# Kernel optimization log

Hardware: AMD Instinct MI355X
Metric: run time of the kernel (lower is better)

The kernel has to match this reference:

```python
import jax, jax.numpy as jnp
import numpy as np

EPS_MIN = 1e-8
N_ITER = 50  # solver_iter


def solve_qp_simplex(M, n_iter=N_ITER):
    """Frank-Wolfe min over the simplex of alpha^T M alpha. M: (B,K,K) -> alpha: (B,K)."""
    B, K, _ = M.shape
    alpha0 = jnp.full((B, K), 1.0 / K, dtype=M.dtype)

    def step(alpha, it):
        grad = 2.0 * jnp.einsum('bij,bj->bi', M, alpha)           # (B,K)
        idx = jnp.argmin(grad, axis=1)                             # (B,)
        s = jax.nn.one_hot(idx, K, dtype=alpha.dtype)              # vertex of simplex
        gamma = 2.0 / (it + 2.0)
        return (1.0 - gamma) * alpha + gamma * s, None

    alpha, _ = jax.lax.scan(step, alpha0, jnp.arange(n_iter, dtype=M.dtype))
    return alpha


def _raw_loss(scores, targets, C):
    B, K = scores.shape
    # epsilon = offdiag_mean of C per batch, scaled by 1.0, clamped
    offdiag_mean = (C.sum(axis=(1, 2)) - jnp.trace(C, axis1=1, axis2=2)) / (K * K - K)
    eps = jnp.maximum(offdiag_mean, EPS_MIN)                       # (B,)

    f = 0.5 * scores
    exponent = -(f[:, :, None] + f[:, None, :] + C) / eps[:, None, None]  # (B,K,K)
    shift = exponent.max(axis=(1, 2), keepdims=True)
    logM = exponent - shift
    M = jnp.exp(logM)

    # solver is an implicit layer: non-differentiable by construction
    alpha = jax.lax.stop_gradient(solve_qp_simplex(M, N_ITER))     # (B,K)

    pos = alpha > 0
    loga = jnp.where(pos, jnp.log(jnp.where(pos, alpha, 1.0)), -jnp.inf)
    term = loga[:, :, None] + loga[:, None, :] + logM              # (B,K,K)
    logval = jax.scipy.special.logsumexp(term.reshape(B, K * K), axis=1)
    conjugate = -eps * (logval + shift.reshape(B))

    f_y = jnp.take_along_axis(scores, targets[:, None], axis=1)[:, 0]
    return conjugate - f_y


def setup_inputs() -> dict:
    key = jax.random.key(0)
    k1, k2, k3 = jax.random.split(key, 3)
    B, K = 512, 256
    scores = jax.random.normal(k1, (B, K), dtype=jnp.float32)
    targets = jax.random.randint(k2, (B,), 0, K)
    C = jax.random.uniform(k3, (B, K, K), dtype=jnp.float32)
    return {"scores": scores, "targets": targets, "C": C}


def reference(scores, targets, C):
    return _raw_loss(scores, targets, C).mean()
```

## Files before the change

### kernel.cpp

```cpp
#include <hip/hip_runtime.h>
#include <math.h>

#define KDIM 256
#define NITER 50


__global__ __launch_bounds__(256) void k1_partials(
    const float* __restrict__ scores, const float* __restrict__ C,
    float* __restrict__ psum_o, float* __restrict__ ptrace_o, float* __restrict__ pmin_o)
{
    const int blk = blockIdx.x;
    const int b = blk >> 2, chunk = blk & 3;
    const int tid = threadIdx.x, lane = tid & 63, wave = tid >> 6;
    const float4* C4 = (const float4*)(C + (size_t)b * KDIM * KDIM);

    __shared__ float4 sf4[KDIM/4];
    __shared__ float redS[256], redT[256], redM[256];
    const float* sf = (const float*)sf4;
    ((float*)sf4)[tid] = 0.5f * scores[b*KDIM + tid];
    __syncthreads();

    const int row0 = chunk * 64;
    float psum = 0.f, ptrace = 0.f, pmin = INFINITY;
    #pragma unroll
    for (int rr = 0; rr < 16; ++rr) {
        const int row = row0 + wave + rr*4;
        float4 c4 = C4[row*(KDIM/4) + lane];
        float frow = sf[row];
        float4 fj = sf4[lane];
        psum += (c4.x + c4.y) + (c4.z + c4.w);
        pmin = fminf(pmin, fminf(fminf(frow+fj.x+c4.x, frow+fj.y+c4.y),
                                 fminf(frow+fj.z+c4.z, frow+fj.w+c4.w)));
        if ((row >> 2) == lane) {
            int r2 = row & 3;
            ptrace += (r2==0) ? c4.x : (r2==1) ? c4.y : (r2==2) ? c4.z : c4.w;
        }
    }
    redS[tid] = psum; redT[tid] = ptrace; redM[tid] = pmin;
    __syncthreads();
    for (int s = 128; s > 0; s >>= 1) {
        if (tid < s) {
            redS[tid] += redS[tid+s];
            redT[tid] += redT[tid+s];
            redM[tid]  = fminf(redM[tid], redM[tid+s]);
        }
        __syncthreads();
    }
    if (tid == 0) { psum_o[blk] = redS[0]; ptrace_o[blk] = redT[0]; pmin_o[blk] = redM[0]; }
}

__global__ __launch_bounds__(256) void k2_grad0(
    const float* __restrict__ scores, const float* __restrict__ C,
    const float* __restrict__ psum_i, const float* __restrict__ ptrace_i, const float* __restrict__ pmin_i,
    float* __restrict__ rsval_o, int* __restrict__ rsidx_o)
{
    const int blk = blockIdx.x;
    const int b = blk >> 2, chunk = blk & 3;
    const int tid = threadIdx.x, lane = tid & 63, wave = tid >> 6;
    const float4* C4 = (const float4*)(C + (size_t)b * KDIM * KDIM);

    __shared__ float4 sf4[KDIM/4];
    __shared__ float rs64[64];
    const float* sf = (const float*)sf4;
    ((float*)sf4)[tid] = 0.5f * scores[b*KDIM + tid];
    __syncthreads();

    float sum = 0.f, tr = 0.f, mn = INFINITY;
    #pragma unroll
    for (int c2 = 0; c2 < 4; ++c2) {
        sum += psum_i[b*4 + c2];
        tr  += ptrace_i[b*4 + c2];
        mn   = fminf(mn, pmin_i[b*4 + c2]);
    }
    const float eps = fmaxf((sum - tr) / (float)(KDIM*KDIM - KDIM), 1e-8f);
    const float inv_eps = 1.0f / eps;
    const float minv = mn;

    const int row0 = chunk * 64;
    for (int rr = wave; rr < 64; rr += 4) {
        const int row = row0 + rr;
        float4 c4 = C4[row*(KDIM/4) + lane];
        float frow = sf[row];
        float4 fj = sf4[lane];
        float p = __expf((minv - (frow+fj.x+c4.x)) * inv_eps)
                + __expf((minv - (frow+fj.y+c4.y)) * inv_eps)
                + __expf((minv - (frow+fj.z+c4.z)) * inv_eps)
                + __expf((minv - (frow+fj.w+c4.w)) * inv_eps);
        for (int off = 32; off > 0; off >>= 1) p += __shfl_xor(p, off);
        if (lane == 0) rs64[rr] = p;
    }
    __syncthreads();
    if (wave == 0) {
        float v = rs64[lane]; int vi = row0 + lane;
        for (int off = 32; off > 0; off >>= 1) {
            float ov = __shfl_xor(v, off);
            int  ovi = __shfl_xor(vi, off);
            if (ov < v || (ov == v && ovi < vi)) { v = ov; vi = ovi; }
        }
        if (lane == 0) { rsval_o[blk] = v; rsidx_o[blk] = vi; }
    }
}

__global__ __launch_bounds__(256) void k3_fw(
    const float* __restrict__ scores, const int* __restrict__ targets,
    const float* __restrict__ C,
    const float* __restrict__ psum_i, const float* __restrict__ ptrace_i, const float* __restrict__ pmin_i,
    const float* __restrict__ rsval_i, const int* __restrict__ rsidx_i,
    float* __restrict__ lossB)
{
    const int b = blockIdx.x;
    const int tid = threadIdx.x, lane = tid & 63, wave = tid >> 6;
    const float* Cb = C + (size_t)b * KDIM * KDIM;

    __shared__ float4 sf4[KDIM/4];
    __shared__ float red[KDIM];
    __shared__ float rs[KDIM];
    __shared__ float wmin[4];
    __shared__ int   widx[4];
    __shared__ int   wcnt[4];
    __shared__ int   sIdx[64];
    __shared__ float sLog[64];

    const float* sf = (const float*)sf4;
    ((float*)sf4)[tid] = 0.5f * scores[b*KDIM + tid];
    __syncthreads();

    float sum = 0.f, tr = 0.f, mn = INFINITY;
    #pragma unroll
    for (int c2 = 0; c2 < 4; ++c2) {
        sum += psum_i[b*4 + c2];
        tr  += ptrace_i[b*4 + c2];
        mn   = fminf(mn, pmin_i[b*4 + c2]);
    }
    const float eps = fmaxf((sum - tr) / (float)(KDIM*KDIM - KDIM), 1e-8f);
    const float inv_eps = 1.0f / eps;
    const float minv = mn;

    float bv = INFINITY; int idx0 = 0;
    #pragma unroll
    for (int c2 = 0; c2 < 4; ++c2) {
        float v = rsval_i[b*4 + c2];
        int  vi = rsidx_i[b*4 + c2];
        if (v < bv) { bv = v; idx0 = vi; }
    }

    const float fi = sf[tid];
    float a = (tid == idx0) ? 1.0f : 0.0f;
    {
        const float c = Cb[tid*KDIM + idx0];
        float dummy; (void)dummy;
        a = a;
    }
    float g;
    {
        const float c = Cb[tid*KDIM + idx0];
        g = 2.0f * __expf((minv - (fi + sf[idx0] + c)) * inv_eps);
    }

    for (int it = 1; it < NITER; ++it) {
        float v = g; int vi = tid;
        for (int off = 32; off > 0; off >>= 1) {
            float ov = __shfl_xor(v, off);
            int  ovi = __shfl_xor(vi, off);
            if (ov < v || (ov == v && ovi < vi)) { v = ov; vi = ovi; }
        }
        if (lane == 0) { wmin[wave] = v; widx[wave] = vi; }
        __syncthreads();
        float cbv = wmin[0]; int cbi = widx[0];
        #pragma unroll
        for (int w = 1; w < 4; ++w) {
            float wv = wmin[w]; int wi = widx[w];
            if (wv < cbv || (wv == cbv && wi < cbi)) { cbv = wv; cbi = wi; }
        }
        const int idx = cbi;
        const float gamma = 2.0f / ((float)it + 2.0f);
        const float fidx = sf[idx];
        const float c = Cb[tid*KDIM + idx];
        const float mcol = __expf((minv - (fi + fidx + c)) * inv_eps);
        g = (1.0f - gamma)*g + 2.0f*gamma*mcol;
        a = (1.0f - gamma)*a + ((tid == idx) ? gamma : 0.0f);
        __syncthreads();
    }

    unsigned long long mask = __ballot(a > 0.f);
    if (lane == 0) wcnt[wave] = __popcll(mask);
    __syncthreads();
    int off0 = 0;
    for (int w = 0; w < wave; ++w) off0 += wcnt[w];
    const int count = wcnt[0] + wcnt[1] + wcnt[2] + wcnt[3];
    if (a > 0.f) {
        int pos = off0 + __popcll(mask & ((1ull << lane) - 1ull));
        sIdx[pos] = tid;
        sLog[pos] = logf(a);
    }
    __syncthreads();

    float m = -INFINITY, ss = 0.f;
    const int total = count * count;
    for (int p = tid; p < total; p += KDIM) {
        int ii = p / count;
        int jj = p - ii * count;
        int i = sIdx[ii], j = sIdx[jj];
        float cij = Cb[i*KDIM + j];
        float lm = (minv - (sf[i] + sf[j] + cij)) * inv_eps;
        float t = sLog[ii] + sLog[jj] + lm;
        if (t > m) { ss = ss * __expf(m - t) + 1.0f; m = t; }
        else       { ss += __expf(t - m); }
    }
    red[tid] = m; rs[tid] = ss;
    __syncthreads();
    for (int s = 128; s > 0; s >>= 1) {
        if (tid < s) {
            float m1 = red[tid],   s1 = rs[tid];
            float m2 = red[tid+s], s2 = rs[tid+s];
            if (s2 > 0.f) {
                if (s1 <= 0.f)    { red[tid] = m2; rs[tid] = s2; }
                else if (m2 > m1) { red[tid] = m2; rs[tid] = s1*__expf(m1-m2) + s2; }
                else              { rs[tid] = s1 + s2*__expf(m2-m1); }
            }
        }
        __syncthreads();
    }
    if (tid == 0) {
        float logval = red[0] + logf(rs[0]);
        float shift = -minv * inv_eps;
        float conjugate = -eps * (logval + shift);
        float fy = scores[b*KDIM + targets[b]];
        lossB[b] = conjugate - fy;
    }
}

__global__ __launch_bounds__(512) void cacis_reduce(const float* __restrict__ lossB,
                                                    float* __restrict__ out, int B)
{
    __shared__ float red[512];
    int t = threadIdx.x;
    red[t] = (t < B) ? lossB[t] : 0.f;
    __syncthreads();
    for (int s = 256; s > 0; s >>= 1) { if (t < s) red[t] += red[t+s]; __syncthreads(); }
    if (t == 0) out[0] = red[0] / (float)B;
}

extern "C" void kernel_launch(void* const* d_in, const int* in_sizes, int n_in,
                              void* d_out, int out_size, void* d_ws, size_t ws_size,
                              hipStream_t stream) {
    const float* scores  = (const float*)d_in[0];
    const int*   targets = (const int*)d_in[1];
    const float* C       = (const float*)d_in[2];
    float* out = (float*)d_out;
    const int B = in_sizes[1];

    float* ws     = (float*)d_ws;
    float* psum   = ws;
    float* ptrace = ws + 2048;
    float* pmin   = ws + 4096;
    float* rsval  = ws + 6144;
    int*   rsidx  = (int*)(ws + 8192);
    float* lossB  = ws + 10240;

    k1_partials<<<B*4, 256, 0, stream>>>(scores, C, psum, ptrace, pmin);
    k2_grad0   <<<B*4, 256, 0, stream>>>(scores, C, psum, ptrace, pmin, rsval, rsidx);
    k3_fw      <<<B,   256, 0, stream>>>(scores, targets, C, psum, ptrace, pmin, rsval, rsidx, lossB);
    cacis_reduce<<<1, 512, 0, stream>>>(lossB, out, B);
}
```

Baseline: 121.4 us.

## Run Frank-Wolfe loop in a single wave and use shuffle-based logsumexp reduction

The 49-iteration Frank-Wolfe loop now runs in one 64-lane wave, with each lane holding four rows. The per-iteration argmin needs only wave shuffles, which removes two block-wide barriers and the shared-memory cross-wave step from every iteration. The final logsumexp merge also switches from a shared-memory tree with eight barriers to wave shuffles plus a single cross-wave combine. The cost is that each lane issues four scattered column loads and four exps per iteration, and the other three waves sit idle during the loop.

```diff
diff --git a/kernel.cpp b/kernel.cpp
--- a/kernel.cpp
+++ b/kernel.cpp
@@ -113,10 +113,8 @@
     const float* Cb = C + (size_t)b * KDIM * KDIM;
 
     __shared__ float4 sf4[KDIM/4];
-    __shared__ float red[KDIM];
-    __shared__ float rs[KDIM];
-    __shared__ float wmin[4];
-    __shared__ int   widx[4];
+    __shared__ float aAll[KDIM];
+    __shared__ float wm[4], wsm[4];
     __shared__ int   wcnt[4];
     __shared__ int   sIdx[64];
     __shared__ float sLog[64];
@@ -144,43 +142,56 @@
         if (v < bv) { bv = v; idx0 = vi; }
     }
 
-    const float fi = sf[tid];
-    float a = (tid == idx0) ? 1.0f : 0.0f;
-    {
-        const float c = Cb[tid*KDIM + idx0];
-        float dummy; (void)dummy;
-        a = a;
-    }
-    float g;
-    {
-        const float c = Cb[tid*KDIM + idx0];
-        g = 2.0f * __expf((minv - (fi + sf[idx0] + c)) * inv_eps);
-    }
-
-    for (int it = 1; it < NITER; ++it) {
-        float v = g; int vi = tid;
-        for (int off = 32; off > 0; off >>= 1) {
-            float ov = __shfl_xor(v, off);
-            int  ovi = __shfl_xor(vi, off);
-            if (ov < v || (ov == v && ovi < vi)) { v = ov; vi = ovi; }
-        }
-        if (lane == 0) { wmin[wave] = v; widx[wave] = vi; }
-        __syncthreads();
-        float cbv = wmin[0]; int cbi = widx[0];
-        #pragma unroll
-        for (int w = 1; w < 4; ++w) {
-            float wv = wmin[w]; int wi = widx[w];
-            if (wv < cbv || (wv == cbv && wi < cbi)) { cbv = wv; cbi = wi; }
-        }
-        const int idx = cbi;
-        const float gamma = 2.0f / ((float)it + 2.0f);
-        const float fidx = sf[idx];
-        const float c = Cb[tid*KDIM + idx];
-        const float mcol = __expf((minv - (fi + fidx + c)) * inv_eps);
-        g = (1.0f - gamma)*g + 2.0f*gamma*mcol;
-        a = (1.0f - gamma)*a + ((tid == idx) ? gamma : 0.0f);
-        __syncthreads();
-    }
+    if (wave == 0) {
+        const float f0 = sf[lane], f1 = sf[lane+64], f2 = sf[lane+128], f3 = sf[lane+192];
+        const float* r0 = Cb + (size_t)lane*KDIM;
+        const float* r1 = r0 + 64*KDIM;
+        const float* r2 = r0 + 128*KDIM;
+        const float* r3 = r0 + 192*KDIM;
+
+        float fidx = sf[idx0];
+        float g0 = 2.0f * __expf((minv - (f0 + fidx + r0[idx0])) * inv_eps);
+        float g1 = 2.0f * __expf((minv - (f1 + fidx + r1[idx0])) * inv_eps);
+        float g2 = 2.0f * __expf((minv - (f2 + fidx + r2[idx0])) * inv_eps);
+        float g3 = 2.0f * __expf((minv - (f3 + fidx + r3[idx0])) * inv_eps);
+        float a0 = (lane     == idx0) ? 1.0f : 0.0f;
+        float a1 = (lane+64  == idx0) ? 1.0f : 0.0f;
+        float a2 = (lane+128 == idx0) ? 1.0f : 0.0f;
+        float a3 = (lane+192 == idx0) ? 1.0f : 0.0f;
+
+        for (int it = 1; it < NITER; ++it) {
+            float v = g0; int vi = lane;
+            if (g1 < v) { v = g1; vi = lane+64; }
+            if (g2 < v) { v = g2; vi = lane+128; }
+            if (g3 < v) { v = g3; vi = lane+192; }
+            #pragma unroll
+            for (int off = 32; off > 0; off >>= 1) {
+                float ov = __shfl_xor(v, off);
+                int  ovi = __shfl_xor(vi, off);
+                if (ov < v || (ov == v && ovi < vi)) { v = ov; vi = ovi; }
+            }
+            const int idx = vi;
+            const float gamma = 2.0f / ((float)it + 2.0f);
+            const float omg = 1.0f - gamma;
+            fidx = sf[idx];
+            const float c0 = r0[idx], c1 = r1[idx], c2_ = r2[idx], c3 = r3[idx];
+            g0 = omg*g0 + 2.0f*gamma*__expf((minv - (f0 + fidx + c0)) * inv_eps);
+            g1 = omg*g1 + 2.0f*gamma*__expf((minv - (f1 + fidx + c1)) * inv_eps);
+            g2 = omg*g2 + 2.0f*gamma*__expf((minv - (f2 + fidx + c2_)) * inv_eps);
+            g3 = omg*g3 + 2.0f*gamma*__expf((minv - (f3 + fidx + c3)) * inv_eps);
+            a0 = omg*a0 + ((lane     == idx) ? gamma : 0.0f);
+            a1 = omg*a1 + ((lane+64  == idx) ? gamma : 0.0f);
+            a2 = omg*a2 + ((lane+128 == idx) ? gamma : 0.0f);
+            a3 = omg*a3 + ((lane+192 == idx) ? gamma : 0.0f);
+        }
+        aAll[lane]     = a0;
+        aAll[lane+64]  = a1;
+        aAll[lane+128] = a2;
+        aAll[lane+192] = a3;
+    }
+    __syncthreads();
+
+    const float a = aAll[tid];
 
     unsigned long long mask = __ballot(a > 0.f);
     if (lane == 0) wcnt[wave] = __popcll(mask);
@@ -207,22 +218,30 @@
         if (t > m) { ss = ss * __expf(m - t) + 1.0f; m = t; }
         else       { ss += __expf(t - m); }
     }
-    red[tid] = m; rs[tid] = ss;
-    __syncthreads();
-    for (int s = 128; s > 0; s >>= 1) {
-        if (tid < s) {
-            float m1 = red[tid],   s1 = rs[tid];
-            float m2 = red[tid+s], s2 = rs[tid+s];
-            if (s2 > 0.f) {
-                if (s1 <= 0.f)    { red[tid] = m2; rs[tid] = s2; }
-                else if (m2 > m1) { red[tid] = m2; rs[tid] = s1*__expf(m1-m2) + s2; }
-                else              { rs[tid] = s1 + s2*__expf(m2-m1); }
+    #pragma unroll
+    for (int off = 32; off > 0; off >>= 1) {
+        float om = __shfl_xor(m, off);
+        float os = __shfl_xor(ss, off);
+        if (os > 0.f) {
+            if (ss <= 0.f)   { m = om; ss = os; }
+            else if (om > m) { ss = ss*__expf(m-om) + os; m = om; }
+            else             { ss += os*__expf(om-m); }
+        }
+    }
+    if (lane == 0) { wm[wave] = m; wsm[wave] = ss; }
+    __syncthreads();
+    if (tid == 0) {
+        float M = wm[0], S = wsm[0];
+        #pragma unroll
+        for (int w = 1; w < 4; ++w) {
+            float om = wm[w], os = wsm[w];
+            if (os > 0.f) {
+                if (S <= 0.f)    { M = om; S = os; }
+                else if (om > M) { S = S*__expf(M-om) + os; M = om; }
+                else             { S += os*__expf(om-M); }
             }
         }
-        __syncthreads();
-    }
-    if (tid == 0) {
-        float logval = red[0] + logf(rs[0]);
+        float logval = M + logf(S);
         float shift = -minv * inv_eps;
         float conjugate = -eps * (logval + shift);
         float fy = scores[b*KDIM + targets[b]];
```

Result: faster. 112.1 us (-7.6%).
